# Optimization experiments

Hardware: AMD Instinct MI355X
Metric: run time of the kernel (lower is better)

## Reference

```python
import jax, jax.numpy as jnp
import numpy as np

GROUPSIZE = 128

def _unpack_int4(packed, axis):
    # packed: int32 array; unpack 8 nibbles per int32 along `axis`.
    shifts = (jnp.arange(8, dtype=jnp.int32) * 4)
    expanded = jnp.expand_dims(packed, axis + 1)  # [..., P, 1, ...]
    shp = [1] * expanded.ndim
    shp[axis + 1] = 8
    nib = (expanded >> shifts.reshape(shp)) & 0xF
    new_shape = list(packed.shape)
    new_shape[axis] = packed.shape[axis] * 8
    return nib.reshape(new_shape)

def setup_inputs() -> dict:
    key = jax.random.key(0)
    k1, k2, k3, k4, k5 = jax.random.split(key, 5)
    in_f, out_f = 4096, 4096
    n_tokens = 8192
    n_groups = in_f // GROUPSIZE
    x = jax.random.normal(k1, (n_tokens, in_f), dtype=jnp.float32)
    qweight = jax.random.randint(k2, (in_f // 8, out_f), 0, 2147483647, dtype=jnp.int32)
    qzeros = jax.random.randint(k3, (n_groups, out_f // 8), 0, 2147483647, dtype=jnp.int32)
    scales = jax.random.uniform(k4, (n_groups, out_f), dtype=jnp.float32) * 0.01
    g_idx = (jnp.arange(in_f, dtype=jnp.int32) // GROUPSIZE).astype(jnp.int32)
    bias = jax.random.normal(k5, (out_f,), dtype=jnp.float32) * 0.01
    return {"x": x, "qweight": qweight, "qzeros": qzeros,
            "scales": scales, "g_idx": g_idx, "bias": bias}

def reference(x, qweight, qzeros, scales, g_idx, bias):
    # Dequantize int4 GPTQ weights: W[k,n] = scales[g_idx[k],n] * (wq[k,n] - (zq[g_idx[k],n]+1))
    wq = _unpack_int4(qweight, axis=0)          # [in, out] int32 nibbles
    zq = _unpack_int4(qzeros, axis=1) + 1       # [n_groups, out]
    scale_k = scales[g_idx]                     # [in, out]
    zero_k = zq[g_idx]                          # [in, out]
    w = scale_k * (wq.astype(x.dtype) - zero_k.astype(x.dtype))  # [in, out]
    return x @ w + bias
```

## Files before the change

kernel.cpp:

```cpp
#include <hip/hip_runtime.h>

typedef __attribute__((ext_vector_type(4))) float  f32x4;
typedef __attribute__((ext_vector_type(8))) short  short8;
typedef __attribute__((ext_vector_type(4))) short  short4v;

#define M_TOK 8192
#define N_OUT 4096
#define K_IN  4096
#define NT    64

typedef const __attribute__((address_space(1))) void* gp_t;
typedef __attribute__((address_space(3))) void* lp_t;
__device__ __forceinline__ void gl_lds16(const void* g, void* l) {
    __builtin_amdgcn_global_load_lds((gp_t)g, (lp_t)l, 16, 0, 0);
}

__global__ __launch_bounds__(256)
void cvt_x(const float* __restrict__ x, unsigned short* __restrict__ xb) {
    const size_t i = ((size_t)blockIdx.x * 256 + threadIdx.x) * 8;
    f32x4 a = *(const f32x4*)(x + i);
    f32x4 b = *(const f32x4*)(x + i + 4);
    union { short8 v; __bf16 h[8]; } u;
    u.h[0] = (__bf16)a.x; u.h[1] = (__bf16)a.y; u.h[2] = (__bf16)a.z; u.h[3] = (__bf16)a.w;
    u.h[4] = (__bf16)b.x; u.h[5] = (__bf16)b.y; u.h[6] = (__bf16)b.z; u.h[7] = (__bf16)b.w;
    *(short8*)(xb + i) = u.v;
}

__global__ __launch_bounds__(256)
void dequant_w(const int* __restrict__ qweight, const int* __restrict__ qzeros,
               const float* __restrict__ scales, unsigned short* __restrict__ Wt) {
    const int k0 = blockIdx.x * 64;
    const int n0 = blockIdx.y * 64;
    const int t  = threadIdx.x;
    const int n  = t & 63;
    const int pl = t >> 6;
    const int g  = k0 >> 7;
    const int ncol = n0 + n;

    const float scale = scales[g * N_OUT + ncol];
    const int qz  = qzeros[g * (N_OUT / 8) + (ncol >> 3)];
    const int zp1 = ((qz >> ((ncol & 7) * 4)) & 0xF) + 1;
    const float zs = -(float)zp1 * scale;

    __shared__ unsigned short wt[64][80];

    const int p0 = k0 >> 3;
    #pragma unroll
    for (int i = 0; i < 2; ++i) {
        const int p_local = pl + i * 4;
        const int q = qweight[(size_t)(p0 + p_local) * N_OUT + ncol];
        union { short8 v; __bf16 h[8]; } u;
        #pragma unroll
        for (int j = 0; j < 8; ++j)
            u.h[j] = (__bf16)fmaf((float)((q >> (4 * j)) & 0xF), scale, zs);
        *(short8*)(&wt[n][8 * p_local]) = u.v;
    }
    __syncthreads();

    #pragma unroll
    for (int it = 0; it < 2; ++it) {
        const int row   = (t >> 3) + 32 * it;
        const int chunk = t & 7;
        short8 v = *(const short8*)(&wt[row][chunk * 8]);
        *(short8*)(Wt + (size_t)(n0 + row) * K_IN + k0 + chunk * 8) = v;
    }
}

__global__ __launch_bounds__(512, 2)
void gemm_bf16_ph(const unsigned short* __restrict__ xb,
                  const unsigned short* __restrict__ Wt,
                  const float* __restrict__ bias,
                  float* __restrict__ out)
{
    const int tid  = threadIdx.x;
    const int lane = tid & 63;
    const int wid  = tid >> 6;
    const int wm   = wid >> 2;
    const int wn   = wid & 3;

    const int bid = blockIdx.x;
    const int swz = (bid & 7) * 64 + (bid >> 3);
    const int m0 = (swz >> 4) * 256;
    const int n0 = (swz & 15) * 256;

    __shared__ __align__(16) unsigned char lds[131072];
    unsigned char* Ab = lds;
    unsigned char* Bb = lds + 65536;

    f32x4 acc[8][4];
    #pragma unroll
    for (int i = 0; i < 8; ++i)
        #pragma unroll
        for (int j = 0; j < 4; ++j)
            acc[i][j] = f32x4{0.f, 0.f, 0.f, 0.f};

    const int sw8    = ((tid & 7) ^ ((tid >> 3) & 7)) * 8;
    const int a_srow = tid >> 3;
    const int b_srow = (wid >> 2) * 64 + (wid & 3) * 8 + (lane >> 3);
    const int a_dst  = wid * 1024;
    const int b_dst  = (wid >> 2) * 8192 + (wid & 3) * 1024;

    const int col0 = (((lane >> 4))     ^ (lane & 7)) << 4;
    const int col1 = ((4 | (lane >> 4)) ^ (lane & 7)) << 4;
    const int arow = (wm * 128 + (lane & 15)) * 128;
    const int brow = (wn * 64  + (lane & 15)) * 128;

    short8 af[4][2], b0[2][2], b1[2][2];

#define CFENCE asm volatile("" ::: "memory")

#define STAGE_A(SEL, KT, H) do { \
    _Pragma("unroll") for (int j_ = 0; j_ < 2; ++j_) \
        gl_lds16(xb + (size_t)(m0 + j_ * 128 + (H) * 64 + a_srow) * K_IN + (KT) * 64 + sw8, \
                 Ab + (SEL) * 32768 + j_ * 16384 + (H) * 8192 + a_dst); } while (0)

#define STAGE_B(SEL, KT, H) do { \
    _Pragma("unroll") for (int j_ = 0; j_ < 2; ++j_) \
        gl_lds16(Wt + (size_t)(n0 + j_ * 128 + (H) * 32 + b_srow) * K_IN + (KT) * 64 + sw8, \
                 Bb + (SEL) * 32768 + j_ * 16384 + (H) * 4096 + b_dst); } while (0)

#define LOAD_A(SEL, HM) do { \
    _Pragma("unroll") for (int mi_ = 0; mi_ < 4; ++mi_) { \
        af[mi_][0] = *(const short8*)(Ab + (SEL) * 32768 + arow + (HM) * 8192 + mi_ * 2048 + col0); \
        af[mi_][1] = *(const short8*)(Ab + (SEL) * 32768 + arow + (HM) * 8192 + mi_ * 2048 + col1); } } while (0)

#define LOAD_B(DST, SEL, HN) do { \
    _Pragma("unroll") for (int ni_ = 0; ni_ < 2; ++ni_) { \
        DST[ni_][0] = *(const short8*)(Bb + (SEL) * 32768 + brow + (HN) * 4096 + ni_ * 2048 + col0); \
        DST[ni_][1] = *(const short8*)(Bb + (SEL) * 32768 + brow + (HN) * 4096 + ni_ * 2048 + col1); } } while (0)

#define MFMA_Q(HM, HN, BF) do { \
    _Pragma("unroll") for (int mi_ = 0; mi_ < 4; ++mi_) \
    _Pragma("unroll") for (int ni_ = 0; ni_ < 2; ++ni_) \
    _Pragma("unroll") for (int kk_ = 0; kk_ < 2; ++kk_) \
        acc[(HM) * 4 + mi_][(HN) * 2 + ni_] = __builtin_amdgcn_mfma_f32_16x16x32_bf16( \
            af[mi_][kk_], BF[ni_][kk_], acc[(HM) * 4 + mi_][(HN) * 2 + ni_], 0, 0, 0); } while (0)

#define K_STEP(CUR, NXT) do { \
     \
    LOAD_A(CUR, 0); \
    LOAD_B(b0, CUR, 0); \
    CFENCE; \
    STAGE_A(NXT, ktn, 0); \
    STAGE_B(NXT, ktn, 0); \
    asm volatile("s_waitcnt vmcnt(6)" ::: "memory"); \
    __builtin_amdgcn_s_barrier(); \
    asm volatile("s_waitcnt lgkmcnt(0)" ::: "memory"); \
    __builtin_amdgcn_sched_barrier(0); \
    __builtin_amdgcn_s_setprio(1); \
    MFMA_Q(0, 0, b0); \
    __builtin_amdgcn_s_setprio(0); \
     \
    LOAD_B(b1, CUR, 1); \
    CFENCE; \
    STAGE_B(NXT, ktn, 1); \
    asm volatile("s_waitcnt vmcnt(6)" ::: "memory"); \
    __builtin_amdgcn_s_barrier(); \
    asm volatile("s_waitcnt lgkmcnt(0)" ::: "memory"); \
    __builtin_amdgcn_sched_barrier(0); \
    __builtin_amdgcn_s_setprio(1); \
    MFMA_Q(0, 1, b1); \
    __builtin_amdgcn_s_setprio(0); \
     \
    LOAD_A(CUR, 1); \
    CFENCE; \
    STAGE_A(NXT, ktn, 1); \
    __builtin_amdgcn_s_barrier(); \
    asm volatile("s_waitcnt lgkmcnt(0)" ::: "memory"); \
    __builtin_amdgcn_sched_barrier(0); \
    __builtin_amdgcn_s_setprio(1); \
    MFMA_Q(1, 0, b0); \
    __builtin_amdgcn_s_setprio(0); \
     \
    asm volatile("s_waitcnt vmcnt(4)" ::: "memory"); \
    __builtin_amdgcn_s_barrier(); \
    __builtin_amdgcn_sched_barrier(0); \
    __builtin_amdgcn_s_setprio(1); \
    MFMA_Q(1, 1, b1); \
    __builtin_amdgcn_s_setprio(0); \
} while (0)

    STAGE_A(0, 0, 0);
    CFENCE;
    STAGE_B(0, 0, 0);
    CFENCE;
    STAGE_B(0, 0, 1);
    CFENCE;
    STAGE_A(0, 0, 1);
    asm volatile("s_waitcnt vmcnt(4)" ::: "memory");
    __builtin_amdgcn_s_barrier();

    int ktn;
    #pragma unroll 1
    for (int kt = 0; kt < NT; kt += 2) {
        ktn = kt + 1;
        K_STEP(0, 1);
        ktn = (kt + 2) & (NT - 1);
        K_STEP(1, 0);
    }

#undef STAGE_A
#undef STAGE_B
#undef LOAD_A
#undef LOAD_B
#undef MFMA_Q
#undef K_STEP
#undef CFENCE

    const int col_base = n0 + wn * 64 + (lane & 15);
    const int row_base = m0 + wm * 128 + (lane >> 4) * 4;
    #pragma unroll
    for (int fn = 0; fn < 4; ++fn) {
        const int col = col_base + fn * 16;
        const float bv = bias[col];
        #pragma unroll
        for (int fm = 0; fm < 8; ++fm) {
            #pragma unroll
            for (int r = 0; r < 4; ++r) {
                const int row = row_base + fm * 16 + r;
                out[(size_t)row * N_OUT + col] = acc[fm][fn][r] + bv;
            }
        }
    }
}

__global__ __launch_bounds__(256, 2)
void gptq_gemm_fused(const float* __restrict__ x,
                     const int*   __restrict__ qweight,
                     const int*   __restrict__ qzeros,
                     const float* __restrict__ scales,
                     const float* __restrict__ bias,
                     float*       __restrict__ out)
{
    const int tid  = threadIdx.x;
    const int lane = tid & 63;
    const int wid  = tid >> 6;
    const int wm   = wid >> 1;
    const int wn   = wid & 1;
    const int m0 = blockIdx.y * 128;
    const int n0 = blockIdx.x * 128;

    __shared__ __align__(16) unsigned char lds[32768];
    unsigned char* Ab = lds;
    unsigned char* Bb = lds + 16384;

    const int ar  = tid >> 4;
    const int ac4 = (tid & 15) * 4;
    const int bnn = tid & 127;
    const int bph = tid >> 7;
    const int ncol = n0 + bnn;

    f32x4 a_reg[8];
    int   q_reg[4];
    float scale_r = 0.f, zs_r = 0.f;

    f32x4 acc[4][4];
    #pragma unroll
    for (int i = 0; i < 4; ++i)
        #pragma unroll
        for (int j = 0; j < 4; ++j)
            acc[i][j] = f32x4{0.f, 0.f, 0.f, 0.f};

    auto load_tile = [&](int kt) {
        const int k0 = kt * 64;
        #pragma unroll
        for (int i = 0; i < 8; ++i)
            a_reg[i] = *(const f32x4*)(x + (size_t)(m0 + ar + 16 * i) * K_IN + k0 + ac4);
        const int p0 = k0 >> 3;
        #pragma unroll
        for (int i = 0; i < 4; ++i)
            q_reg[i] = qweight[(size_t)(p0 + i * 2 + bph) * N_OUT + ncol];
        const int g = k0 >> 7;
        scale_r = scales[g * N_OUT + ncol];
        const int qz = qzeros[g * (N_OUT / 8) + (ncol >> 3)];
        zs_r = -(float)(((qz >> ((ncol & 7) * 4)) & 0xF) + 1) * scale_r;
    };

    auto store_tile = [&]() {
        #pragma unroll
        for (int i = 0; i < 8; ++i) {
            const int r = ar + 16 * i;
            const int addr = r * 128 + ((ac4 * 2) ^ ((r & 7) << 4));
            union { short4v v; __bf16 h[4]; } u;
            u.h[0] = (__bf16)a_reg[i].x; u.h[1] = (__bf16)a_reg[i].y;
            u.h[2] = (__bf16)a_reg[i].z; u.h[3] = (__bf16)a_reg[i].w;
            *(short4v*)(Ab + addr) = u.v;
        }
        #pragma unroll
        for (int i = 0; i < 4; ++i) {
            const int pl = i * 2 + bph;
            const int q  = q_reg[i];
            union { short8 v; __bf16 h[8]; } u;
            #pragma unroll
            for (int j = 0; j < 8; ++j)
                u.h[j] = (__bf16)fmaf((float)((q >> (4 * j)) & 0xF), scale_r, zs_r);
            const int addr = bnn * 128 + ((pl * 16) ^ ((bnn & 7) << 4));
            *(short8*)(Bb + addr) = u.v;
        }
    };

    auto compute_tile = [&]() {
        #pragma unroll
        for (int kk = 0; kk < 2; ++kk) {
            short8 afr[4], bfr[4];
            const int cb = kk * 64 + (lane >> 4) * 16;
            #pragma unroll
            for (int mi = 0; mi < 4; ++mi) {
                const int r = wm * 64 + mi * 16 + (lane & 15);
                afr[mi] = *(const short8*)(Ab + r * 128 + (cb ^ ((r & 7) << 4)));
            }
            #pragma unroll
            for (int ni = 0; ni < 4; ++ni) {
                const int nn = wn * 64 + ni * 16 + (lane & 15);
                bfr[ni] = *(const short8*)(Bb + nn * 128 + (cb ^ ((nn & 7) << 4)));
            }
            #pragma unroll
            for (int mi = 0; mi < 4; ++mi)
                #pragma unroll
                for (int ni = 0; ni < 4; ++ni)
                    acc[mi][ni] = __builtin_amdgcn_mfma_f32_16x16x32_bf16(
                        afr[mi], bfr[ni], acc[mi][ni], 0, 0, 0);
        }
    };

    load_tile(0);
    for (int kt = 0; kt < NT; ++kt) {
        if (kt) __syncthreads();
        store_tile();
        __syncthreads();
        if (kt + 1 < NT) load_tile(kt + 1);
        compute_tile();
    }

    const int col_base = n0 + wn * 64 + (lane & 15);
    const int row_base = m0 + wm * 64 + (lane >> 4) * 4;
    #pragma unroll
    for (int ni = 0; ni < 4; ++ni) {
        const int col = col_base + ni * 16;
        const float bv = bias[col];
        #pragma unroll
        for (int mi = 0; mi < 4; ++mi)
            #pragma unroll
            for (int r = 0; r < 4; ++r)
                out[(size_t)(row_base + mi * 16 + r) * N_OUT + col] = acc[mi][ni][r] + bv;
    }
}

extern "C" void kernel_launch(void* const* d_in, const int* in_sizes, int n_in,
                              void* d_out, int out_size, void* d_ws, size_t ws_size,
                              hipStream_t stream) {
    const float* x       = (const float*)d_in[0];
    const int*   qweight = (const int*)  d_in[1];
    const int*   qzeros  = (const int*)  d_in[2];
    const float* scales  = (const float*)d_in[3];
    const float* bias    = (const float*)d_in[5];
    float* out = (float*)d_out;

    const size_t xb_bytes = (size_t)M_TOK * K_IN * 2;
    const size_t wt_bytes = (size_t)N_OUT * K_IN * 2;

    if (ws_size >= xb_bytes + wt_bytes) {
        unsigned short* xb = (unsigned short*)d_ws;
        unsigned short* Wt = (unsigned short*)((char*)d_ws + xb_bytes);
        cvt_x<<<dim3((M_TOK * K_IN) / (256 * 8)), dim3(256), 0, stream>>>(x, xb);
        dequant_w<<<dim3(K_IN / 64, N_OUT / 64), dim3(256), 0, stream>>>(qweight, qzeros, scales, Wt);
        gemm_bf16_ph<<<dim3((M_TOK / 256) * (N_OUT / 256)), dim3(512), 0, stream>>>(xb, Wt, bias, out);
    } else {
        gptq_gemm_fused<<<dim3(N_OUT / 128, M_TOK / 128), dim3(256), 0, stream>>>(
            x, qweight, qzeros, scales, bias, out);
    }
}
```

Measured before the change: 255.8 us.

## Double-buffer register fragments and prefetch next tile's LDS reads during MFMA

```diff
diff --git a/kernel.cpp b/kernel.cpp
--- a/kernel.cpp
+++ b/kernel.cpp
@@ -67,7 +67,7 @@
 }
 
 __global__ __launch_bounds__(512, 2)
-void gemm_bf16_ph(const unsigned short* __restrict__ xb,
+void gemm_bf16_dp(const unsigned short* __restrict__ xb,
                   const unsigned short* __restrict__ Wt,
                   const float* __restrict__ bias,
                   float* __restrict__ out)
@@ -105,7 +105,7 @@
     const int arow = (wm * 128 + (lane & 15)) * 128;
     const int brow = (wn * 64  + (lane & 15)) * 128;
 
-    short8 af[4][2], b0[2][2], b1[2][2];
+    short8 afA[4][2], afB[4][2], b0[2][2], b1[2][2];
 
 #define CFENCE asm volatile("" ::: "memory")
 
@@ -119,64 +119,64 @@
         gl_lds16(Wt + (size_t)(n0 + j_ * 128 + (H) * 32 + b_srow) * K_IN + (KT) * 64 + sw8, \
                  Bb + (SEL) * 32768 + j_ * 16384 + (H) * 4096 + b_dst); } while (0)
 
-#define LOAD_A(SEL, HM) do { \
+#define LOAD_A(DST, SEL, HM) do { \
     _Pragma("unroll") for (int mi_ = 0; mi_ < 4; ++mi_) { \
-        af[mi_][0] = *(const short8*)(Ab + (SEL) * 32768 + arow + (HM) * 8192 + mi_ * 2048 + col0); \
-        af[mi_][1] = *(const short8*)(Ab + (SEL) * 32768 + arow + (HM) * 8192 + mi_ * 2048 + col1); } } while (0)
+        DST[mi_][0] = *(const short8*)(Ab + (SEL) * 32768 + arow + (HM) * 8192 + mi_ * 2048 + col0); \
+        DST[mi_][1] = *(const short8*)(Ab + (SEL) * 32768 + arow + (HM) * 8192 + mi_ * 2048 + col1); } } while (0)
 
 #define LOAD_B(DST, SEL, HN) do { \
     _Pragma("unroll") for (int ni_ = 0; ni_ < 2; ++ni_) { \
         DST[ni_][0] = *(const short8*)(Bb + (SEL) * 32768 + brow + (HN) * 4096 + ni_ * 2048 + col0); \
         DST[ni_][1] = *(const short8*)(Bb + (SEL) * 32768 + brow + (HN) * 4096 + ni_ * 2048 + col1); } } while (0)
 
-#define MFMA_Q(HM, HN, BF) do { \
+#define MFMA_Q(HM, HN, AF, BF) do { \
     _Pragma("unroll") for (int mi_ = 0; mi_ < 4; ++mi_) \
     _Pragma("unroll") for (int ni_ = 0; ni_ < 2; ++ni_) \
     _Pragma("unroll") for (int kk_ = 0; kk_ < 2; ++kk_) \
         acc[(HM) * 4 + mi_][(HN) * 2 + ni_] = __builtin_amdgcn_mfma_f32_16x16x32_bf16( \
-            af[mi_][kk_], BF[ni_][kk_], acc[(HM) * 4 + mi_][(HN) * 2 + ni_], 0, 0, 0); } while (0)
+            AF[mi_][kk_], BF[ni_][kk_], acc[(HM) * 4 + mi_][(HN) * 2 + ni_], 0, 0, 0); } while (0)
 
 #define K_STEP(CUR, NXT) do { \
      \
-    LOAD_A(CUR, 0); \
-    LOAD_B(b0, CUR, 0); \
-    CFENCE; \
     STAGE_A(NXT, ktn, 0); \
     STAGE_B(NXT, ktn, 0); \
-    asm volatile("s_waitcnt vmcnt(6)" ::: "memory"); \
+    STAGE_B(NXT, ktn, 1); \
+    STAGE_A(NXT, ktn, 1); \
+    asm volatile("s_waitcnt vmcnt(8)" ::: "memory"); \
     __builtin_amdgcn_s_barrier(); \
+    CFENCE; \
+    LOAD_B(b1, CUR, 1); \
+    asm volatile("s_waitcnt lgkmcnt(4)" ::: "memory"); \
+    __builtin_amdgcn_sched_barrier(0); \
+    __builtin_amdgcn_s_setprio(1); \
+    MFMA_Q(0, 0, afA, b0); \
+    __builtin_amdgcn_s_setprio(0); \
+     \
+    __builtin_amdgcn_s_barrier(); \
+    CFENCE; \
+    LOAD_A(afB, CUR, 1); \
+    asm volatile("s_waitcnt lgkmcnt(8)" ::: "memory"); \
+    __builtin_amdgcn_sched_barrier(0); \
+    __builtin_amdgcn_s_setprio(1); \
+    MFMA_Q(0, 1, afA, b1); \
+    __builtin_amdgcn_s_setprio(0); \
+     \
+    __builtin_amdgcn_s_barrier(); \
+    CFENCE; \
     asm volatile("s_waitcnt lgkmcnt(0)" ::: "memory"); \
     __builtin_amdgcn_sched_barrier(0); \
     __builtin_amdgcn_s_setprio(1); \
-    MFMA_Q(0, 0, b0); \
-    __builtin_amdgcn_s_setprio(0); \
-     \
-    LOAD_B(b1, CUR, 1); \
-    CFENCE; \
-    STAGE_B(NXT, ktn, 1); \
-    asm volatile("s_waitcnt vmcnt(6)" ::: "memory"); \
-    __builtin_amdgcn_s_barrier(); \
-    asm volatile("s_waitcnt lgkmcnt(0)" ::: "memory"); \
-    __builtin_amdgcn_sched_barrier(0); \
-    __builtin_amdgcn_s_setprio(1); \
-    MFMA_Q(0, 1, b1); \
-    __builtin_amdgcn_s_setprio(0); \
-     \
-    LOAD_A(CUR, 1); \
-    CFENCE; \
-    STAGE_A(NXT, ktn, 1); \
-    __builtin_amdgcn_s_barrier(); \
-    asm volatile("s_waitcnt lgkmcnt(0)" ::: "memory"); \
-    __builtin_amdgcn_sched_barrier(0); \
-    __builtin_amdgcn_s_setprio(1); \
-    MFMA_Q(1, 0, b0); \
+    MFMA_Q(1, 0, afB, b0); \
     __builtin_amdgcn_s_setprio(0); \
      \
     asm volatile("s_waitcnt vmcnt(4)" ::: "memory"); \
     __builtin_amdgcn_s_barrier(); \
-    __builtin_amdgcn_sched_barrier(0); \
+    CFENCE; \
+    LOAD_A(afA, NXT, 0); \
+    LOAD_B(b0, NXT, 0); \
+    CFENCE; \
     __builtin_amdgcn_s_setprio(1); \
-    MFMA_Q(1, 1, b1); \
+    MFMA_Q(1, 1, afB, b1); \
     __builtin_amdgcn_s_setprio(0); \
 } while (0)
 
@@ -189,6 +189,9 @@
     STAGE_A(0, 0, 1);
     asm volatile("s_waitcnt vmcnt(4)" ::: "memory");
     __builtin_amdgcn_s_barrier();
+    CFENCE;
+    LOAD_A(afA, 0, 0);
+    LOAD_B(b0, 0, 0);
 
     int ktn;
     #pragma unroll 1
@@ -324,11 +327,11 @@
     };
 
     load_tile(0);
-    for (int kt = 0; kt < NT; ++kt) {
+    for (int kt = 0; kt < 64; ++kt) {
         if (kt) __syncthreads();
         store_tile();
         __syncthreads();
-        if (kt + 1 < NT) load_tile(kt + 1);
+        if (kt + 1 < 64) load_tile(kt + 1);
         compute_tile();
     }
 
@@ -364,7 +367,7 @@
         unsigned short* Wt = (unsigned short*)((char*)d_ws + xb_bytes);
         cvt_x<<<dim3((M_TOK * K_IN) / (256 * 8)), dim3(256), 0, stream>>>(x, xb);
         dequant_w<<<dim3(K_IN / 64, N_OUT / 64), dim3(256), 0, stream>>>(qweight, qzeros, scales, Wt);
-        gemm_bf16_ph<<<dim3((M_TOK / 256) * (N_OUT / 256)), dim3(512), 0, stream>>>(xb, Wt, bias, out);
+        gemm_bf16_dp<<<dim3((M_TOK / 256) * (N_OUT / 256)), dim3(512), 0, stream>>>(xb, Wt, bias, out);
     } else {
         gptq_gemm_fused<<<dim3(N_OUT / 128, M_TOK / 128), dim3(256), 0, stream>>>(
             x, qweight, qzeros, scales, bias, out);
```

Result: slower. 380.0 us (+48.6%).

## Fuse fp32-to-bf16 conversion of activations into GEMM A-tile staging

Applied to the files above, without the earlier changes.

```diff
diff --git a/kernel.cpp b/kernel.cpp
--- a/kernel.cpp
+++ b/kernel.cpp
@@ -13,17 +13,6 @@
 typedef __attribute__((address_space(3))) void* lp_t;
 __device__ __forceinline__ void gl_lds16(const void* g, void* l) {
     __builtin_amdgcn_global_load_lds((gp_t)g, (lp_t)l, 16, 0, 0);
-}
-
-__global__ __launch_bounds__(256)
-void cvt_x(const float* __restrict__ x, unsigned short* __restrict__ xb) {
-    const size_t i = ((size_t)blockIdx.x * 256 + threadIdx.x) * 8;
-    f32x4 a = *(const f32x4*)(x + i);
-    f32x4 b = *(const f32x4*)(x + i + 4);
-    union { short8 v; __bf16 h[8]; } u;
-    u.h[0] = (__bf16)a.x; u.h[1] = (__bf16)a.y; u.h[2] = (__bf16)a.z; u.h[3] = (__bf16)a.w;
-    u.h[4] = (__bf16)b.x; u.h[5] = (__bf16)b.y; u.h[6] = (__bf16)b.z; u.h[7] = (__bf16)b.w;
-    *(short8*)(xb + i) = u.v;
 }
 
 __global__ __launch_bounds__(256)
@@ -67,7 +56,7 @@
 }
 
 __global__ __launch_bounds__(512, 2)
-void gemm_bf16_ph(const unsigned short* __restrict__ xb,
+void gemm_bf16_fx(const float* __restrict__ x,
                   const unsigned short* __restrict__ Wt,
                   const float* __restrict__ bias,
                   float* __restrict__ out)
@@ -97,7 +86,6 @@
     const int sw8    = ((tid & 7) ^ ((tid >> 3) & 7)) * 8;
     const int a_srow = tid >> 3;
     const int b_srow = (wid >> 2) * 64 + (wid & 3) * 8 + (lane >> 3);
-    const int a_dst  = wid * 1024;
     const int b_dst  = (wid >> 2) * 8192 + (wid & 3) * 1024;
 
     const int col0 = (((lane >> 4))     ^ (lane & 7)) << 4;
@@ -106,13 +94,24 @@
     const int brow = (wn * 64  + (lane & 15)) * 128;
 
     short8 af[4][2], b0[2][2], b1[2][2];
+    f32x4 ra0[2][2], ra1[2][2];
 
 #define CFENCE asm volatile("" ::: "memory")
 
-#define STAGE_A(SEL, KT, H) do { \
+#define LOADX(RA, KT, H) do { \
     _Pragma("unroll") for (int j_ = 0; j_ < 2; ++j_) \
-        gl_lds16(xb + (size_t)(m0 + j_ * 128 + (H) * 64 + a_srow) * K_IN + (KT) * 64 + sw8, \
-                 Ab + (SEL) * 32768 + j_ * 16384 + (H) * 8192 + a_dst); } while (0)
+    _Pragma("unroll") for (int q_ = 0; q_ < 2; ++q_) \
+        RA[j_][q_] = *(const f32x4*)(x + (size_t)(m0 + j_ * 128 + (H) * 64 + a_srow) * K_IN \
+                                       + (KT) * 64 + sw8 + q_ * 4); } while (0)
+
+#define CVTW(RA, SEL, H) do { \
+    _Pragma("unroll") for (int j_ = 0; j_ < 2; ++j_) { \
+        union { short8 v; __bf16 h[8]; } u_; \
+        u_.h[0] = (__bf16)RA[j_][0].x; u_.h[1] = (__bf16)RA[j_][0].y; \
+        u_.h[2] = (__bf16)RA[j_][0].z; u_.h[3] = (__bf16)RA[j_][0].w; \
+        u_.h[4] = (__bf16)RA[j_][1].x; u_.h[5] = (__bf16)RA[j_][1].y; \
+        u_.h[6] = (__bf16)RA[j_][1].z; u_.h[7] = (__bf16)RA[j_][1].w; \
+        *(short8*)(Ab + (SEL) * 32768 + j_ * 16384 + (H) * 8192 + tid * 16) = u_.v; } } while (0)
 
 #define STAGE_B(SEL, KT, H) do { \
     _Pragma("unroll") for (int j_ = 0; j_ < 2; ++j_) \
@@ -141,9 +140,8 @@
     LOAD_A(CUR, 0); \
     LOAD_B(b0, CUR, 0); \
     CFENCE; \
-    STAGE_A(NXT, ktn, 0); \
+    LOADX(ra0, ktn, 0); \
     STAGE_B(NXT, ktn, 0); \
-    asm volatile("s_waitcnt vmcnt(6)" ::: "memory"); \
     __builtin_amdgcn_s_barrier(); \
     asm volatile("s_waitcnt lgkmcnt(0)" ::: "memory"); \
     __builtin_amdgcn_sched_barrier(0); \
@@ -153,8 +151,10 @@
      \
     LOAD_B(b1, CUR, 1); \
     CFENCE; \
+    CVTW(ra0, NXT, 0); \
+    CFENCE; \
+    LOADX(ra1, ktn, 1); \
     STAGE_B(NXT, ktn, 1); \
-    asm volatile("s_waitcnt vmcnt(6)" ::: "memory"); \
     __builtin_amdgcn_s_barrier(); \
     asm volatile("s_waitcnt lgkmcnt(0)" ::: "memory"); \
     __builtin_amdgcn_sched_barrier(0); \
@@ -164,7 +164,7 @@
      \
     LOAD_A(CUR, 1); \
     CFENCE; \
-    STAGE_A(NXT, ktn, 1); \
+    CVTW(ra1, NXT, 1); \
     __builtin_amdgcn_s_barrier(); \
     asm volatile("s_waitcnt lgkmcnt(0)" ::: "memory"); \
     __builtin_amdgcn_sched_barrier(0); \
@@ -172,7 +172,7 @@
     MFMA_Q(1, 0, b0); \
     __builtin_amdgcn_s_setprio(0); \
      \
-    asm volatile("s_waitcnt vmcnt(4)" ::: "memory"); \
+    asm volatile("s_waitcnt vmcnt(0)" ::: "memory"); \
     __builtin_amdgcn_s_barrier(); \
     __builtin_amdgcn_sched_barrier(0); \
     __builtin_amdgcn_s_setprio(1); \
@@ -180,14 +180,15 @@
     __builtin_amdgcn_s_setprio(0); \
 } while (0)
 
-    STAGE_A(0, 0, 0);
+    LOADX(ra0, 0, 0);
+    LOADX(ra1, 0, 1);
     CFENCE;
     STAGE_B(0, 0, 0);
-    CFENCE;
     STAGE_B(0, 0, 1);
     CFENCE;
-    STAGE_A(0, 0, 1);
-    asm volatile("s_waitcnt vmcnt(4)" ::: "memory");
+    CVTW(ra0, 0, 0);
+    CVTW(ra1, 0, 1);
+    asm volatile("s_waitcnt vmcnt(0) lgkmcnt(0)" ::: "memory");
     __builtin_amdgcn_s_barrier();
 
     int ktn;
@@ -199,7 +200,8 @@
         K_STEP(1, 0);
     }
 
-#undef STAGE_A
+#undef LOADX
+#undef CVTW
 #undef STAGE_B
 #undef LOAD_A
 #undef LOAD_B
@@ -324,11 +326,11 @@
     };
 
     load_tile(0);
-    for (int kt = 0; kt < NT; ++kt) {
+    for (int kt = 0; kt < 64; ++kt) {
         if (kt) __syncthreads();
         store_tile();
         __syncthreads();
-        if (kt + 1 < NT) load_tile(kt + 1);
+        if (kt + 1 < 64) load_tile(kt + 1);
         compute_tile();
     }
 
@@ -356,15 +358,12 @@
     const float* bias    = (const float*)d_in[5];
     float* out = (float*)d_out;
 
-    const size_t xb_bytes = (size_t)M_TOK * K_IN * 2;
     const size_t wt_bytes = (size_t)N_OUT * K_IN * 2;
 
-    if (ws_size >= xb_bytes + wt_bytes) {
-        unsigned short* xb = (unsigned short*)d_ws;
-        unsigned short* Wt = (unsigned short*)((char*)d_ws + xb_bytes);
-        cvt_x<<<dim3((M_TOK * K_IN) / (256 * 8)), dim3(256), 0, stream>>>(x, xb);
+    if (ws_size >= wt_bytes) {
+        unsigned short* Wt = (unsigned short*)d_ws;
         dequant_w<<<dim3(K_IN / 64, N_OUT / 64), dim3(256), 0, stream>>>(qweight, qzeros, scales, Wt);
-        gemm_bf16_ph<<<dim3((M_TOK / 256) * (N_OUT / 256)), dim3(512), 0, stream>>>(xb, Wt, bias, out);
+        gemm_bf16_fx<<<dim3((M_TOK / 256) * (N_OUT / 256)), dim3(512), 0, stream>>>(x, Wt, bias, out);
     } else {
         gptq_gemm_fused<<<dim3(N_OUT / 128, M_TOK / 128), dim3(256), 0, stream>>>(
             x, qweight, qzeros, scales, bias, out);
```

Result: slower. 400.2 us (+56.4%).
